# Kernel optimization log

Hardware: AMD Instinct MI355X
Metric: run time of the kernel (lower is better)

Reference implementation:

```python
import jax, jax.numpy as jnp
import numpy as np

N, IN_DIM, H1, H2, LIN, MAX_INDEX = 16384, 64, 256, 256, 64, 256


def _init_layer(key, out_dim, in_dim):
    # mimic kaiming_uniform(a=sqrt(5)) + uniform bias bound = 1/sqrt(fan_in)
    kW, kb = jax.random.split(key)
    bound_w = 1.0 / np.sqrt(in_dim)  # gain*sqrt(3/fan_in) with a=sqrt(5) -> 1/sqrt(fan_in)
    W = jax.random.uniform(kW, (MAX_INDEX, out_dim, in_dim), jnp.float32, -bound_w, bound_w)
    b = jax.random.uniform(kb, (MAX_INDEX, out_dim), jnp.float32, -bound_w, bound_w)
    return W, b


def setup_inputs() -> dict:
    key = jax.random.key(0)
    kx, ki, k1, k2, k3 = jax.random.split(key, 5)
    x = jax.random.normal(kx, (N, IN_DIM), jnp.float32)
    ind = jax.random.randint(ki, (N,), 0, MAX_INDEX, jnp.int64 if jax.config.jax_enable_x64 else jnp.int32)
    W1, b1 = _init_layer(k1, H1, IN_DIM)
    W2, b2 = _init_layer(k2, H2, H1)
    Wl, bl = _init_layer(k3, LIN, H2)
    return {"x": x, "ind": ind, "W1": W1, "b1": b1, "W2": W2, "b2": b2, "Wl": Wl, "bl": bl}


def _index_linear(x, ind, W, b):
    # per-row expert weight gather then row-wise matvec: out[n] = W[ind[n]] @ x[n] + b[ind[n]]
    return jnp.einsum('noi,ni->no', W[ind], x) + b[ind]


def reference(x, ind, W1, b1, W2, b2, Wl, bl):
    h = jnp.tanh(_index_linear(x, ind, W1, b1))
    h = jnp.tanh(_index_linear(h, ind, W2, b2))
    return _index_linear(h, ind, Wl, bl)
```

## Files before the change

kernel.cpp:

```cpp
#include <hip/hip_runtime.h>
#include <math.h>

#define NROWS   16384
#define IN_DIM  64
#define HID     256
#define OUT_DIM 64
#define NEXP    256
#define MT      112
#define NT      7
#define HP      264

typedef __attribute__((ext_vector_type(8))) short short8;
typedef __attribute__((ext_vector_type(4))) float f32x4;
typedef __attribute__((ext_vector_type(4))) unsigned uint4v;
typedef __attribute__((ext_vector_type(2))) unsigned uint2v;


__global__ __launch_bounds__(256) void hist_k(const int* __restrict__ ind,
                                              int* __restrict__ hist) {
  int n = blockIdx.x * 256 + threadIdx.x;
  atomicAdd(&hist[ind[n]], 1);
}

__global__ __launch_bounds__(256) void scan_k(const int* __restrict__ hist,
                                              int* __restrict__ offsets,
                                              int* __restrict__ cur) {
  __shared__ int s[NEXP];
  int t = threadIdx.x;
  int h = hist[t];
  s[t] = h;
  __syncthreads();
  for (int d = 1; d < NEXP; d <<= 1) {
    int v = (t >= d) ? s[t - d] : 0;
    __syncthreads();
    s[t] += v;
    __syncthreads();
  }
  int exc = s[t] - h;
  offsets[t] = exc;
  cur[t] = exc;
  if (t == NEXP - 1) offsets[NEXP] = s[t];
}

__global__ __launch_bounds__(256) void scatter_k(const int* __restrict__ ind,
                                                 int* __restrict__ cur,
                                                 int* __restrict__ rows) {
  int n = blockIdx.x * 256 + threadIdx.x;
  int p = atomicAdd(&cur[ind[n]], 1);
  rows[p] = n;
}


__device__ __forceinline__ unsigned bf16_rn(float f) {
  unsigned u = __builtin_bit_cast(unsigned, f);
  unsigned r = 0x7fffu + ((u >> 16) & 1u);
  return (u + r) >> 16;
}

__device__ __forceinline__ unsigned pk2(float a, float b) {
  return bf16_rn(a) | (bf16_rn(b) << 16);
}

__device__ __forceinline__ short8 cvt8(f32x4 w0, f32x4 w1) {
  uint4v u;
  u.x = pk2(w0.x, w0.y);
  u.y = pk2(w0.z, w0.w);
  u.z = pk2(w1.x, w1.y);
  u.w = pk2(w1.z, w1.w);
  return __builtin_bit_cast(short8, u);
}

__device__ __forceinline__ float fast_tanh(float v) {
  float e = __expf(2.f * v);
  return 1.f - 2.f * __builtin_amdgcn_rcpf(e + 1.f);
}

template <int CPRL>
__device__ __forceinline__ void stage_slice(const float* __restrict__ g, int krow,
                                            int colbase, float* l, int t) {
#pragma unroll
  for (int r = 0; r < 4; r++) {
    int c = r * 512 + t;
    int row = c >> CPRL;
    int cin = c & ((1 << CPRL) - 1);
    const float* src = g + (size_t)row * krow + colbase + cin * 4;
    __builtin_amdgcn_global_load_lds(
        (const __attribute__((address_space(1))) void*)src,
        (__attribute__((address_space(3))) void*)(l + (size_t)c * 4), 16, 0, 0);
  }
}

__device__ __forceinline__ void slice_mm(const float* Ws, const unsigned short* Hin,
                                         int hofs, int w, int l15, int q,
                                         f32x4 (&acc)[2][NT]) {
  short8 a[2];
#pragma unroll
  for (int mt = 0; mt < 2; mt++) {
    const float* ap = Ws + (w * 32 + mt * 16 + l15) * 32 + q * 8;
    a[mt] = cvt8(*(const f32x4*)ap, *(const f32x4*)(ap + 4));
  }
#pragma unroll
  for (int nt = 0; nt < NT; nt++) {
    short8 b = *(const short8*)&Hin[(nt * 16 + l15) * HP + hofs + q * 8];
#pragma unroll
    for (int mt = 0; mt < 2; mt++)
      acc[mt][nt] =
          __builtin_amdgcn_mfma_f32_16x16x32_bf16(a[mt], b, acc[mt][nt], 0, 0, 0);
  }
}

__device__ __forceinline__ void slice_l3(const float* Ws, const unsigned short* Hin,
                                         int ks2, int w, int l15, int q,
                                         f32x4 (&accl)[4]) {
#pragma unroll
  for (int kk = 0; kk < 4; kk++) {
    const float* ap = Ws + ((w & 3) * 16 + l15) * 128 + kk * 32 + q * 8;
    short8 a = cvt8(*(const f32x4*)ap, *(const f32x4*)(ap + 4));
    int hofs = ks2 * 128 + kk * 32;
#pragma unroll
    for (int i = 0; i < 4; i++) {
      int nt = (w >> 2) * 4 + i;
      if (nt < NT) {
        short8 b = *(const short8*)&Hin[(nt * 16 + l15) * HP + hofs + q * 8];
        accl[i] = __builtin_amdgcn_mfma_f32_16x16x32_bf16(a, b, accl[i], 0, 0, 0);
      }
    }
  }
}

__device__ __forceinline__ void write_h8(f32x4 (&acc)[2][NT], unsigned short* Hd,
                                         int w, int l15, int q) {
#pragma unroll
  for (int mt = 0; mt < 2; mt++)
#pragma unroll
    for (int nt = 0; nt < NT; nt++) {
      uint2v v;
      v.x = pk2(fast_tanh(acc[mt][nt].x), fast_tanh(acc[mt][nt].y));
      v.y = pk2(fast_tanh(acc[mt][nt].z), fast_tanh(acc[mt][nt].w));
      *(uint2v*)&Hd[(nt * 16 + l15) * HP + w * 32 + mt * 16 + q * 4] = v;
    }
}


__global__ __launch_bounds__(512, 2) void mlp_k(
    const float* __restrict__ x,
    const float* __restrict__ W1, const float* __restrict__ b1,
    const float* __restrict__ W2, const float* __restrict__ b2,
    const float* __restrict__ Wl, const float* __restrict__ bl,
    const int* __restrict__ rows, const int* __restrict__ offsets,
    float* __restrict__ out) {
  __shared__ __align__(16) unsigned short H[MT * HP];
  __shared__ __align__(16) float Wb[2][8192];

  const int t = threadIdx.x;
  const int w = t >> 6;
  const int l15 = t & 15;
  const int q = (t >> 4) & 3;
  const int e = blockIdx.x;
  const int beg = offsets[e];
  const int cnt = offsets[e + 1] - beg;

  const float* W1e = W1 + (size_t)e * HID * IN_DIM;
  const float* W2e = W2 + (size_t)e * HID * HID;
  const float* Wle = Wl + (size_t)e * OUT_DIM * HID;

  f32x4 b1v[2], b2v[2], blv;
#pragma unroll
  for (int mt = 0; mt < 2; mt++) {
    b1v[mt] = *(const f32x4*)(b1 + (size_t)e * HID + w * 32 + mt * 16 + q * 4);
    b2v[mt] = *(const f32x4*)(b2 + (size_t)e * HID + w * 32 + mt * 16 + q * 4);
  }
  blv = *(const f32x4*)(bl + (size_t)e * OUT_DIM + (w & 3) * 16 + q * 4);

  const int sr = t >> 2;
  const int sc = (t & 3) * 16;

  for (int mt0 = 0; mt0 < cnt; mt0 += MT) {
    stage_slice<3>(W1e, IN_DIM, 0, Wb[0], t);
    if (sr < MT) {
      int gm = mt0 + sr;
      bool val = gm < cnt;
      int r = val ? rows[beg + gm] : 0;
      const float* xr = x + (size_t)r * IN_DIM + sc;
      uint4v u0, u1;
      if (val) {
        f32x4 a0 = *(const f32x4*)(xr);
        f32x4 a1 = *(const f32x4*)(xr + 4);
        f32x4 a2 = *(const f32x4*)(xr + 8);
        f32x4 a3 = *(const f32x4*)(xr + 12);
        u0.x = pk2(a0.x, a0.y); u0.y = pk2(a0.z, a0.w);
        u0.z = pk2(a1.x, a1.y); u0.w = pk2(a1.z, a1.w);
        u1.x = pk2(a2.x, a2.y); u1.y = pk2(a2.z, a2.w);
        u1.z = pk2(a3.x, a3.y); u1.w = pk2(a3.z, a3.w);
      } else {
        u0 = (uint4v){0, 0, 0, 0};
        u1 = (uint4v){0, 0, 0, 0};
      }
      *(uint4v*)&H[sr * HP + sc] = u0;
      *(uint4v*)&H[sr * HP + sc + 8] = u1;
    }
    __syncthreads();

    f32x4 acc[2][NT];
#pragma unroll
    for (int mt = 0; mt < 2; mt++)
#pragma unroll
      for (int nt = 0; nt < NT; nt++) acc[mt][nt] = b1v[mt];

    stage_slice<3>(W1e, IN_DIM, 32, Wb[1], t);
    slice_mm(Wb[0], H, 0, w, l15, q, acc);
    __syncthreads();

    stage_slice<3>(W2e, HID, 0, Wb[0], t);
    slice_mm(Wb[1], H, 32, w, l15, q, acc);
    __syncthreads();

    write_h8(acc, H, w, l15, q);
    __syncthreads();

#pragma unroll
    for (int mt = 0; mt < 2; mt++)
#pragma unroll
      for (int nt = 0; nt < NT; nt++) acc[mt][nt] = b2v[mt];

    for (int ks = 0; ks < 8; ks++) {
      if (ks < 7) stage_slice<3>(W2e, HID, (ks + 1) * 32, Wb[(ks + 1) & 1], t);
      else        stage_slice<5>(Wle, HID, 0, Wb[0], t);
      slice_mm(Wb[ks & 1], H, ks * 32, w, l15, q, acc);
      __syncthreads();
    }

    write_h8(acc, H, w, l15, q);
    __syncthreads();

    f32x4 accl[4];
#pragma unroll
    for (int i = 0; i < 4; i++) accl[i] = blv;

    stage_slice<5>(Wle, HID, 128, Wb[1], t);
    slice_l3(Wb[0], H, 0, w, l15, q, accl);
    __syncthreads();
    slice_l3(Wb[1], H, 1, w, l15, q, accl);

#pragma unroll
    for (int i = 0; i < 4; i++) {
      int nt = (w >> 2) * 4 + i;
      if (nt < NT) {
        int gm = mt0 + nt * 16 + l15;
        if (gm < cnt) {
          int r = rows[beg + gm];
          *(f32x4*)(out + (size_t)r * OUT_DIM + (w & 3) * 16 + q * 4) = accl[i];
        }
      }
    }
    __syncthreads();
  }
}


extern "C" void kernel_launch(void* const* d_in, const int* in_sizes, int n_in,
                              void* d_out, int out_size, void* d_ws, size_t ws_size,
                              hipStream_t stream) {
  const float* x   = (const float*)d_in[0];
  const int*   ind = (const int*)d_in[1];
  const float* W1  = (const float*)d_in[2];
  const float* b1  = (const float*)d_in[3];
  const float* W2  = (const float*)d_in[4];
  const float* b2  = (const float*)d_in[5];
  const float* Wl  = (const float*)d_in[6];
  const float* bl  = (const float*)d_in[7];
  float* out = (float*)d_out;

  int* offsets = (int*)d_ws;
  int* cur     = (int*)d_ws + 260;
  int* hist    = (int*)d_ws + 260;
  int* rows    = (int*)d_ws + 516;

  hipMemsetAsync(hist, 0, NEXP * sizeof(int), stream);
  hist_k<<<NROWS / 256, 256, 0, stream>>>(ind, hist);
  scan_k<<<1, 256, 0, stream>>>(hist, offsets, cur);
  scatter_k<<<NROWS / 256, 256, 0, stream>>>(ind, cur, rows);
  mlp_k<<<NEXP, 512, 0, stream>>>(x, W1, b1, W2, b2, Wl, bl, rows, offsets, out);
}
```

Measured before the change: 164.7 us.

## Deepen weight-slice prefetch pipeline with vmcnt barriers and XOR-swizzle LDS layout

Replaces __syncthreads with explicit s_waitcnt vmcnt(4) plus s_barrier so two async global-to-LDS weight slices stay in flight, prefetching two slices ahead instead of one. The x-row loads are hoisted ahead of the W1 staging. It also XOR-swizzles the staged weight layout to reduce LDS bank conflicts on the A-fragment reads. Relying on hand-counted vmcnt and barriers without full fences risks races if the count of outstanding loads per thread does not match.

Measured after the change: 164.4 us. No clear change (-0.2%).

```diff
diff --git a/kernel.cpp b/kernel.cpp
--- a/kernel.cpp
+++ b/kernel.cpp
@@ -14,6 +14,15 @@
 typedef __attribute__((ext_vector_type(4))) float f32x4;
 typedef __attribute__((ext_vector_type(4))) unsigned uint4v;
 typedef __attribute__((ext_vector_type(2))) unsigned uint2v;
+
+#define WAITVM4_BAR() do { \
+    asm volatile("s_waitcnt vmcnt(4) lgkmcnt(0)" ::: "memory"); \
+    __builtin_amdgcn_s_barrier(); } while (0)
+#define WAITVM0_BAR() do { \
+    asm volatile("s_waitcnt vmcnt(0) lgkmcnt(0)" ::: "memory"); \
+    __builtin_amdgcn_s_barrier(); } while (0)
+#define RBAR() __builtin_amdgcn_s_barrier()
+#define MEMFENCE() asm volatile("" ::: "memory")
 
 
 __global__ __launch_bounds__(256) void hist_k(const int* __restrict__ ind,
@@ -81,8 +90,9 @@
 #pragma unroll
   for (int r = 0; r < 4; r++) {
     int c = r * 512 + t;
-    int row = c >> CPRL;
-    int cin = c & ((1 << CPRL) - 1);
+    int cs = c ^ ((c >> CPRL) & 7);
+    int row = cs >> CPRL;
+    int cin = cs & ((1 << CPRL) - 1);
     const float* src = g + (size_t)row * krow + colbase + cin * 4;
     __builtin_amdgcn_global_load_lds(
         (const __attribute__((address_space(1))) void*)src,
@@ -93,11 +103,14 @@
 __device__ __forceinline__ void slice_mm(const float* Ws, const unsigned short* Hin,
                                          int hofs, int w, int l15, int q,
                                          f32x4 (&acc)[2][NT]) {
+  const int xa = (l15 & 7) << 2;
+  const int c0 = (q * 8) ^ xa;
+  const int c1 = (q * 8 + 4) ^ xa;
   short8 a[2];
 #pragma unroll
   for (int mt = 0; mt < 2; mt++) {
-    const float* ap = Ws + (w * 32 + mt * 16 + l15) * 32 + q * 8;
-    a[mt] = cvt8(*(const f32x4*)ap, *(const f32x4*)(ap + 4));
+    const float* ap = Ws + (w * 32 + mt * 16 + l15) * 32;
+    a[mt] = cvt8(*(const f32x4*)(ap + c0), *(const f32x4*)(ap + c1));
   }
 #pragma unroll
   for (int nt = 0; nt < NT; nt++) {
@@ -112,10 +125,13 @@
 __device__ __forceinline__ void slice_l3(const float* Ws, const unsigned short* Hin,
                                          int ks2, int w, int l15, int q,
                                          f32x4 (&accl)[4]) {
+  const int xa = (l15 & 7) << 2;
+  const int c0 = (q * 8) ^ xa;
+  const int c1 = (q * 8 + 4) ^ xa;
 #pragma unroll
   for (int kk = 0; kk < 4; kk++) {
-    const float* ap = Ws + ((w & 3) * 16 + l15) * 128 + kk * 32 + q * 8;
-    short8 a = cvt8(*(const f32x4*)ap, *(const f32x4*)(ap + 4));
+    const float* ap = Ws + ((w & 3) * 16 + l15) * 128 + kk * 32;
+    short8 a = cvt8(*(const f32x4*)(ap + c0), *(const f32x4*)(ap + c1));
     int hofs = ks2 * 128 + kk * 32;
 #pragma unroll
     for (int i = 0; i < 4; i++) {
@@ -176,18 +192,28 @@
   const int sc = (t & 3) * 16;
 
   for (int mt0 = 0; mt0 < cnt; mt0 += MT) {
-    stage_slice<3>(W1e, IN_DIM, 0, Wb[0], t);
+    f32x4 a0, a1, a2, a3;
+    bool val = false;
     if (sr < MT) {
       int gm = mt0 + sr;
-      bool val = gm < cnt;
+      val = gm < cnt;
       int r = val ? rows[beg + gm] : 0;
       const float* xr = x + (size_t)r * IN_DIM + sc;
+      if (val) {
+        a0 = *(const f32x4*)(xr);
+        a1 = *(const f32x4*)(xr + 4);
+        a2 = *(const f32x4*)(xr + 8);
+        a3 = *(const f32x4*)(xr + 12);
+      }
+    }
+    MEMFENCE();
+    stage_slice<3>(W1e, IN_DIM, 0, Wb[0], t);
+    MEMFENCE();
+    stage_slice<3>(W1e, IN_DIM, 32, Wb[1], t);
+    MEMFENCE();
+    if (sr < MT) {
       uint4v u0, u1;
       if (val) {
-        f32x4 a0 = *(const f32x4*)(xr);
-        f32x4 a1 = *(const f32x4*)(xr + 4);
-        f32x4 a2 = *(const f32x4*)(xr + 8);
-        f32x4 a3 = *(const f32x4*)(xr + 12);
         u0.x = pk2(a0.x, a0.y); u0.y = pk2(a0.z, a0.w);
         u0.z = pk2(a1.x, a1.y); u0.w = pk2(a1.z, a1.w);
         u1.x = pk2(a2.x, a2.y); u1.y = pk2(a2.z, a2.w);
@@ -199,7 +225,6 @@
       *(uint4v*)&H[sr * HP + sc] = u0;
       *(uint4v*)&H[sr * HP + sc + 8] = u1;
     }
-    __syncthreads();
 
     f32x4 acc[2][NT];
 #pragma unroll
@@ -207,16 +232,16 @@
 #pragma unroll
       for (int nt = 0; nt < NT; nt++) acc[mt][nt] = b1v[mt];
 
-    stage_slice<3>(W1e, IN_DIM, 32, Wb[1], t);
+    WAITVM4_BAR();
     slice_mm(Wb[0], H, 0, w, l15, q, acc);
-    __syncthreads();
-
+    RBAR();
     stage_slice<3>(W2e, HID, 0, Wb[0], t);
+
+    WAITVM4_BAR();
     slice_mm(Wb[1], H, 32, w, l15, q, acc);
-    __syncthreads();
-
+    RBAR();
+    stage_slice<3>(W2e, HID, 32, Wb[1], t);
     write_h8(acc, H, w, l15, q);
-    __syncthreads();
 
 #pragma unroll
     for (int mt = 0; mt < 2; mt++)
@@ -224,22 +249,26 @@
       for (int nt = 0; nt < NT; nt++) acc[mt][nt] = b2v[mt];
 
     for (int ks = 0; ks < 8; ks++) {
-      if (ks < 7) stage_slice<3>(W2e, HID, (ks + 1) * 32, Wb[(ks + 1) & 1], t);
-      else        stage_slice<5>(Wle, HID, 0, Wb[0], t);
+      WAITVM4_BAR();
       slice_mm(Wb[ks & 1], H, ks * 32, w, l15, q, acc);
-      __syncthreads();
-    }
-
-    write_h8(acc, H, w, l15, q);
-    __syncthreads();
+      RBAR();
+      if (ks < 6) {
+        stage_slice<3>(W2e, HID, (ks + 2) * 32, Wb[ks & 1], t);
+      } else if (ks == 6) {
+        stage_slice<5>(Wle, HID, 0, Wb[0], t);
+      } else {
+        stage_slice<5>(Wle, HID, 128, Wb[1], t);
+        write_h8(acc, H, w, l15, q);
+      }
+    }
 
     f32x4 accl[4];
 #pragma unroll
     for (int i = 0; i < 4; i++) accl[i] = blv;
 
-    stage_slice<5>(Wle, HID, 128, Wb[1], t);
+    WAITVM4_BAR();
     slice_l3(Wb[0], H, 0, w, l15, q, accl);
-    __syncthreads();
+    WAITVM0_BAR();
     slice_l3(Wb[1], H, 1, w, l15, q, accl);
 
 #pragma unroll
@@ -253,7 +282,7 @@
         }
       }
     }
-    __syncthreads();
+    RBAR();
   }
 }
 
```

## Load expert weights directly into registers instead of staging through LDS

Applied to the files above, without the earlier changes.

Removes the LDS double-buffer for the weight slices. Each thread now reads its own MFMA A-operand rows straight from global memory into registers, using a software prefetch pipeline (depth 2 for W1 and Wl, depth 3 for W2), and the first slices are preloaded before the x gather. Most block-wide syncs between K slices are dropped, and the remaining __syncthreads are replaced with an LDS-only wait plus s_barrier. This frees 64KB of shared memory and cuts barrier count, at the cost of more VGPR pressure and uncoalesced, strided per-lane global loads. Weights are also now reloaded per row tile rather than cooperatively staged.

After: 163.5 us. No clear change (-0.7%).

```diff
diff --git a/kernel.cpp b/kernel.cpp
--- a/kernel.cpp
+++ b/kernel.cpp
@@ -14,6 +14,10 @@
 typedef __attribute__((ext_vector_type(4))) float f32x4;
 typedef __attribute__((ext_vector_type(4))) unsigned uint4v;
 typedef __attribute__((ext_vector_type(2))) unsigned uint2v;
+
+#define LBAR() do { \
+    asm volatile("s_waitcnt lgkmcnt(0)" ::: "memory"); \
+    __builtin_amdgcn_s_barrier(); } while (0)
 
 
 __global__ __launch_bounds__(256) void hist_k(const int* __restrict__ ind,
@@ -75,53 +79,91 @@
   return 1.f - 2.f * __builtin_amdgcn_rcpf(e + 1.f);
 }
 
-template <int CPRL>
-__device__ __forceinline__ void stage_slice(const float* __restrict__ g, int krow,
-                                            int colbase, float* l, int t) {
-#pragma unroll
-  for (int r = 0; r < 4; r++) {
-    int c = r * 512 + t;
-    int row = c >> CPRL;
-    int cin = c & ((1 << CPRL) - 1);
-    const float* src = g + (size_t)row * krow + colbase + cin * 4;
-    __builtin_amdgcn_global_load_lds(
-        (const __attribute__((address_space(1))) void*)src,
-        (__attribute__((address_space(3))) void*)(l + (size_t)c * 4), 16, 0, 0);
-  }
-}
-
-__device__ __forceinline__ void slice_mm(const float* Ws, const unsigned short* Hin,
-                                         int hofs, int w, int l15, int q,
-                                         f32x4 (&acc)[2][NT]) {
-  short8 a[2];
-#pragma unroll
-  for (int mt = 0; mt < 2; mt++) {
-    const float* ap = Ws + (w * 32 + mt * 16 + l15) * 32 + q * 8;
-    a[mt] = cvt8(*(const f32x4*)ap, *(const f32x4*)(ap + 4));
-  }
-#pragma unroll
-  for (int nt = 0; nt < NT; nt++) {
-    short8 b = *(const short8*)&Hin[(nt * 16 + l15) * HP + hofs + q * 8];
-#pragma unroll
-    for (int mt = 0; mt < 2; mt++)
-      acc[mt][nt] =
-          __builtin_amdgcn_mfma_f32_16x16x32_bf16(a[mt], b, acc[mt][nt], 0, 0, 0);
-  }
-}
-
-__device__ __forceinline__ void slice_l3(const float* Ws, const unsigned short* Hin,
-                                         int ks2, int w, int l15, int q,
-                                         f32x4 (&accl)[4]) {
-#pragma unroll
-  for (int kk = 0; kk < 4; kk++) {
-    const float* ap = Ws + ((w & 3) * 16 + l15) * 128 + kk * 32 + q * 8;
-    short8 a = cvt8(*(const f32x4*)ap, *(const f32x4*)(ap + 4));
-    int hofs = ks2 * 128 + kk * 32;
+
+__device__ __forceinline__ void preload2(const float* bp0, const float* bp1,
+                                         f32x4 (&p)[2][2]) {
+  p[0][0] = *(const f32x4*)(bp0);
+  p[0][1] = *(const f32x4*)(bp0 + 4);
+  p[1][0] = *(const f32x4*)(bp1);
+  p[1][1] = *(const f32x4*)(bp1 + 4);
+}
+
+__device__ __forceinline__ void layer1_direct(const float* bp0, const float* bp1,
+                                              f32x4 (&pre)[2][2],
+                                              const unsigned short* Hin,
+                                              int l15, int q, f32x4 (&acc)[2][NT]) {
+  f32x4 wp[2][2][2];
+  wp[0][0][0] = pre[0][0]; wp[0][0][1] = pre[0][1];
+  wp[0][1][0] = pre[1][0]; wp[0][1][1] = pre[1][1];
+#pragma unroll
+  for (int ks = 0; ks < 2; ks++) {
+    const int cu = ks & 1;
+    if (ks + 1 < 2) {
+      wp[cu ^ 1][0][0] = *(const f32x4*)(bp0 + (ks + 1) * 32);
+      wp[cu ^ 1][0][1] = *(const f32x4*)(bp0 + (ks + 1) * 32 + 4);
+      wp[cu ^ 1][1][0] = *(const f32x4*)(bp1 + (ks + 1) * 32);
+      wp[cu ^ 1][1][1] = *(const f32x4*)(bp1 + (ks + 1) * 32 + 4);
+    }
+    short8 a0 = cvt8(wp[cu][0][0], wp[cu][0][1]);
+    short8 a1 = cvt8(wp[cu][1][0], wp[cu][1][1]);
+#pragma unroll
+    for (int nt = 0; nt < NT; nt++) {
+      short8 b = *(const short8*)&Hin[(nt * 16 + l15) * HP + ks * 32 + q * 8];
+      acc[0][nt] = __builtin_amdgcn_mfma_f32_16x16x32_bf16(a0, b, acc[0][nt], 0, 0, 0);
+      acc[1][nt] = __builtin_amdgcn_mfma_f32_16x16x32_bf16(a1, b, acc[1][nt], 0, 0, 0);
+    }
+  }
+}
+
+__device__ __forceinline__ void layer2_direct(const float* bp0, const float* bp1,
+                                              f32x4 (&pre)[2][2][2],
+                                              const unsigned short* Hin,
+                                              int l15, int q, f32x4 (&acc)[2][NT]) {
+  f32x4 wp[3][2][2];
+  wp[0][0][0] = pre[0][0][0]; wp[0][0][1] = pre[0][0][1];
+  wp[0][1][0] = pre[0][1][0]; wp[0][1][1] = pre[0][1][1];
+  wp[1][0][0] = pre[1][0][0]; wp[1][0][1] = pre[1][0][1];
+  wp[1][1][0] = pre[1][1][0]; wp[1][1][1] = pre[1][1][1];
+#pragma unroll
+  for (int ks = 0; ks < 8; ks++) {
+    const int cu = ks % 3;
+    const int ld = (ks + 2) % 3;
+    if (ks + 2 < 8) {
+      wp[ld][0][0] = *(const f32x4*)(bp0 + (ks + 2) * 32);
+      wp[ld][0][1] = *(const f32x4*)(bp0 + (ks + 2) * 32 + 4);
+      wp[ld][1][0] = *(const f32x4*)(bp1 + (ks + 2) * 32);
+      wp[ld][1][1] = *(const f32x4*)(bp1 + (ks + 2) * 32 + 4);
+    }
+    short8 a0 = cvt8(wp[cu][0][0], wp[cu][0][1]);
+    short8 a1 = cvt8(wp[cu][1][0], wp[cu][1][1]);
+#pragma unroll
+    for (int nt = 0; nt < NT; nt++) {
+      short8 b = *(const short8*)&Hin[(nt * 16 + l15) * HP + ks * 32 + q * 8];
+      acc[0][nt] = __builtin_amdgcn_mfma_f32_16x16x32_bf16(a0, b, acc[0][nt], 0, 0, 0);
+      acc[1][nt] = __builtin_amdgcn_mfma_f32_16x16x32_bf16(a1, b, acc[1][nt], 0, 0, 0);
+    }
+  }
+}
+
+__device__ __forceinline__ void layer3_direct(const float* bp, f32x4 (&pre)[2],
+                                              const unsigned short* Hin,
+                                              int w, int l15, int q,
+                                              f32x4 (&accl)[4]) {
+  f32x4 wp[2][2];
+  wp[0][0] = pre[0]; wp[0][1] = pre[1];
+#pragma unroll
+  for (int kk = 0; kk < 8; kk++) {
+    const int cu = kk & 1;
+    if (kk + 1 < 8) {
+      wp[cu ^ 1][0] = *(const f32x4*)(bp + (kk + 1) * 32);
+      wp[cu ^ 1][1] = *(const f32x4*)(bp + (kk + 1) * 32 + 4);
+    }
+    short8 a = cvt8(wp[cu][0], wp[cu][1]);
 #pragma unroll
     for (int i = 0; i < 4; i++) {
       int nt = (w >> 2) * 4 + i;
       if (nt < NT) {
-        short8 b = *(const short8*)&Hin[(nt * 16 + l15) * HP + hofs + q * 8];
+        short8 b = *(const short8*)&Hin[(nt * 16 + l15) * HP + kk * 32 + q * 8];
         accl[i] = __builtin_amdgcn_mfma_f32_16x16x32_bf16(a, b, accl[i], 0, 0, 0);
       }
     }
@@ -150,7 +192,6 @@
     const int* __restrict__ rows, const int* __restrict__ offsets,
     float* __restrict__ out) {
   __shared__ __align__(16) unsigned short H[MT * HP];
-  __shared__ __align__(16) float Wb[2][8192];
 
   const int t = threadIdx.x;
   const int w = t >> 6;
@@ -164,6 +205,12 @@
   const float* W2e = W2 + (size_t)e * HID * HID;
   const float* Wle = Wl + (size_t)e * OUT_DIM * HID;
 
+  const float* bp1a = W1e + (size_t)(w * 32 + l15) * IN_DIM + q * 8;
+  const float* bp1b = W1e + (size_t)(w * 32 + 16 + l15) * IN_DIM + q * 8;
+  const float* bp2a = W2e + (size_t)(w * 32 + l15) * HID + q * 8;
+  const float* bp2b = W2e + (size_t)(w * 32 + 16 + l15) * HID + q * 8;
+  const float* bp3  = Wle + (size_t)((w & 3) * 16 + l15) * HID + q * 8;
+
   f32x4 b1v[2], b2v[2], blv;
 #pragma unroll
   for (int mt = 0; mt < 2; mt++) {
@@ -176,7 +223,13 @@
   const int sc = (t & 3) * 16;
 
   for (int mt0 = 0; mt0 < cnt; mt0 += MT) {
-    stage_slice<3>(W1e, IN_DIM, 0, Wb[0], t);
+    f32x4 p1[2][2], p2[2][2][2], p3[2];
+    preload2(bp1a, bp1b, p1);
+    preload2(bp2a, bp2b, p2[0]);
+    preload2(bp2a + 32, bp2b + 32, p2[1]);
+    p3[0] = *(const f32x4*)(bp3);
+    p3[1] = *(const f32x4*)(bp3 + 4);
+
     if (sr < MT) {
       int gm = mt0 + sr;
       bool val = gm < cnt;
@@ -199,48 +252,31 @@
       *(uint4v*)&H[sr * HP + sc] = u0;
       *(uint4v*)&H[sr * HP + sc + 8] = u1;
     }
-    __syncthreads();
+    LBAR();
 
     f32x4 acc[2][NT];
 #pragma unroll
     for (int mt = 0; mt < 2; mt++)
 #pragma unroll
       for (int nt = 0; nt < NT; nt++) acc[mt][nt] = b1v[mt];
-
-    stage_slice<3>(W1e, IN_DIM, 32, Wb[1], t);
-    slice_mm(Wb[0], H, 0, w, l15, q, acc);
-    __syncthreads();
-
-    stage_slice<3>(W2e, HID, 0, Wb[0], t);
-    slice_mm(Wb[1], H, 32, w, l15, q, acc);
-    __syncthreads();
-
+    layer1_direct(bp1a, bp1b, p1, H, l15, q, acc);
+    LBAR();
     write_h8(acc, H, w, l15, q);
-    __syncthreads();
+    LBAR();
 
 #pragma unroll
     for (int mt = 0; mt < 2; mt++)
 #pragma unroll
       for (int nt = 0; nt < NT; nt++) acc[mt][nt] = b2v[mt];
-
-    for (int ks = 0; ks < 8; ks++) {
-      if (ks < 7) stage_slice<3>(W2e, HID, (ks + 1) * 32, Wb[(ks + 1) & 1], t);
-      else        stage_slice<5>(Wle, HID, 0, Wb[0], t);
-      slice_mm(Wb[ks & 1], H, ks * 32, w, l15, q, acc);
-      __syncthreads();
-    }
-
+    layer2_direct(bp2a, bp2b, p2, H, l15, q, acc);
+    LBAR();
     write_h8(acc, H, w, l15, q);
-    __syncthreads();
+    LBAR();
 
     f32x4 accl[4];
 #pragma unroll
     for (int i = 0; i < 4; i++) accl[i] = blv;
-
-    stage_slice<5>(Wle, HID, 128, Wb[1], t);
-    slice_l3(Wb[0], H, 0, w, l15, q, accl);
-    __syncthreads();
-    slice_l3(Wb[1], H, 1, w, l15, q, accl);
+    layer3_direct(bp3, p3, H, w, l15, q, accl);
 
 #pragma unroll
     for (int i = 0; i < 4; i++) {
@@ -253,7 +289,7 @@
         }
       }
     }
-    __syncthreads();
+    LBAR();
   }
 }
 
```
